# Kernel tuning notes

Hardware: AMD Instinct MI355X
Metric: run time of the kernel (lower is better)

The kernel has to match this reference:

```python
import jax, jax.numpy as jnp
import numpy as np

N_NODES = 50000
N_EDGES = 600000
N_GRAPHS = 1024
D = 128
NEG_SLOPE = 0.2


def _gat_conv(x, W, a_src, a_dst, b, src, dst, n):
    # PyG GATConv, heads=1, concat=True, add_self_loops=True (self loops
    # already appended to src/dst by the caller).
    h = x @ W                                  # [N, C]
    alpha_src = h @ a_src                      # [N]
    alpha_dst = h @ a_dst                      # [N]
    e = jax.nn.leaky_relu(alpha_src[src] + alpha_dst[dst], NEG_SLOPE)  # [E']
    # segment softmax over incoming edges of each destination node
    e_max = jax.ops.segment_max(e, dst, num_segments=n)
    ex = jnp.exp(e - e_max[dst])
    denom = jax.ops.segment_sum(ex, dst, num_segments=n)
    alpha = ex / denom[dst]
    out = jax.ops.segment_sum(h[src] * alpha[:, None], dst, num_segments=n)
    return out + b


def _global_mean_pool(x, batch, n_graphs):
    s = jax.ops.segment_sum(x, batch, num_segments=n_graphs)
    cnt = jax.ops.segment_sum(jnp.ones((x.shape[0],), x.dtype), batch,
                              num_segments=n_graphs)
    return s / jnp.maximum(cnt, 1.0)[:, None]


def setup_inputs() -> dict:
    key = jax.random.key(0)
    ks = jax.random.split(key, 12)
    x = jax.random.normal(ks[0], (N_NODES, D), dtype=jnp.float32)
    edge_index = jax.random.randint(ks[1], (2, N_EDGES), 0, N_NODES, dtype=jnp.int64)
    batch = jnp.sort(jax.random.randint(ks[2], (N_NODES,), 0, N_GRAPHS, dtype=jnp.int64))
    glorot = 1.0 / np.sqrt(D)
    return {
        "x": x,
        "edge_index": edge_index,
        "batch": batch,
        "W1": jax.random.normal(ks[3], (D, D), dtype=jnp.float32) * glorot,
        "att_src1": jax.random.normal(ks[4], (D,), dtype=jnp.float32) * glorot,
        "att_dst1": jax.random.normal(ks[5], (D,), dtype=jnp.float32) * glorot,
        "b1": jnp.zeros((D,), dtype=jnp.float32),
        "W2": jax.random.normal(ks[6], (D, D), dtype=jnp.float32) * glorot,
        "att_src2": jax.random.normal(ks[7], (D,), dtype=jnp.float32) * glorot,
        "att_dst2": jax.random.normal(ks[8], (D,), dtype=jnp.float32) * glorot,
        "b2": jnp.zeros((D,), dtype=jnp.float32),
    }


def reference(x, edge_index, batch, W1, att_src1, att_dst1, b1,
              W2, att_src2, att_dst2, b2):
    n = x.shape[0]
    loops = jnp.arange(n, dtype=edge_index.dtype)
    src = jnp.concatenate([edge_index[0], loops])
    dst = jnp.concatenate([edge_index[1], loops])

    h1 = jax.nn.relu(_gat_conv(x, W1, att_src1, att_dst1, b1, src, dst, n))
    emb1 = _global_mean_pool(h1, batch, N_GRAPHS)

    h2 = jax.nn.relu(_gat_conv(h1, W2, att_src2, att_dst2, b2, src, dst, n))
    emb2 = _global_mean_pool(h2, batch, N_GRAPHS)

    return (emb1, emb2)
```

## Files before the change

kernel.cpp:

```cpp
#include <hip/hip_runtime.h>
#include <hip/hip_fp16.h>
#include <cstdint>
#include <cstddef>

#define NN 50000
#define NE 600000
#define NT (NE + NN)
#define NG 1024
#define D 128
#define NEG_SLOPE 0.2f

typedef _Float16 half8 __attribute__((ext_vector_type(8)));
typedef float f32x4 __attribute__((ext_vector_type(4)));

__global__ void prep_misc(const float* __restrict__ W1, const float* __restrict__ W2,
                          _Float16* __restrict__ Wt1, _Float16* __restrict__ Wt2,
                          const int* __restrict__ batch, int* __restrict__ gptr,
                          unsigned* __restrict__ deg) {
    int i = blockIdx.x * 256 + threadIdx.x;
    if (i < NN) deg[i] = 0u;
    if (i < 2 * D * D) {
        const float* W  = (i < D * D) ? W1 : W2;
        _Float16*   Wt  = (i < D * D) ? Wt1 : Wt2;
        int j = i & (D * D - 1);
        int k = j >> 7, c = j & 127;
        Wt[c * D + k] = (_Float16)W[j];
    }
    if (i <= NG) {
        int lo = 0, hi = NN;
        while (lo < hi) { int mid = (lo + hi) >> 1; if (batch[mid] < i) lo = mid + 1; else hi = mid; }
        gptr[i] = lo;
    }
}

__global__ void hist_kernel(const int* __restrict__ ei1, unsigned* __restrict__ deg) {
    int e = blockIdx.x * blockDim.x + threadIdx.x;
    if (e >= NT) return;
    int d = (e < NE) ? ei1[e] : (e - NE);
    atomicAdd(deg + d, 1u);
}

__global__ void scan1(const unsigned* __restrict__ deg, unsigned* __restrict__ chunk,
                      unsigned* __restrict__ partials) {
    __shared__ unsigned sm[256];
    int i = blockIdx.x * 256 + threadIdx.x;
    unsigned v = (i < NN) ? deg[i] : 0u;
    sm[threadIdx.x] = v;
    __syncthreads();
    for (int off = 1; off < 256; off <<= 1) {
        unsigned t = (threadIdx.x >= off) ? sm[threadIdx.x - off] : 0u;
        __syncthreads();
        sm[threadIdx.x] += t;
        __syncthreads();
    }
    if (i < NN) chunk[i] = sm[threadIdx.x];
    if (threadIdx.x == 255) partials[blockIdx.x] = sm[255];
}

__global__ void scan2(unsigned* __restrict__ partials, int nb) {
    __shared__ unsigned sm[256];
    int i = threadIdx.x;
    sm[i] = (i < nb) ? partials[i] : 0u;
    __syncthreads();
    for (int off = 1; off < 256; off <<= 1) {
        unsigned t = (i >= off) ? sm[i - off] : 0u;
        __syncthreads();
        sm[i] += t;
        __syncthreads();
    }
    if (i < nb) partials[i] = sm[i];
}

__global__ void scan3(const unsigned* __restrict__ chunk, const unsigned* __restrict__ deg,
                      const unsigned* __restrict__ pscan, int* __restrict__ ptr,
                      int* __restrict__ fill) {
    int i = blockIdx.x * 256 + threadIdx.x;
    if (i < NN) {
        unsigned off = blockIdx.x ? pscan[blockIdx.x - 1] : 0u;
        int excl = (int)(chunk[i] - deg[i] + off);
        ptr[i] = excl;
        fill[i] = excl;
    }
    if (i == 0) ptr[NN] = NT;
}

__global__ void scatter_kernel(const int* __restrict__ ei0, const int* __restrict__ ei1,
                               int* __restrict__ fill, int* __restrict__ csr_src) {
    int e = blockIdx.x * blockDim.x + threadIdx.x;
    if (e >= NT) return;
    int s, d;
    if (e < NE) { s = ei0[e]; d = ei1[e]; } else { s = d = e - NE; }
    int pos = atomicAdd(fill + d, 1);
    csr_src[pos] = s;
}

template <bool FP16IN>
__global__ __launch_bounds__(256) void gemm_mfma(
    const void* __restrict__ Xv, const _Float16* __restrict__ Wt,
    const float* __restrict__ a_s, const float* __restrict__ a_d,
    __half2* __restrict__ Hh, float* __restrict__ AS, float* __restrict__ AD)
{
    __shared__ _Float16 Ht[64][132];
    int t = threadIdx.x;
    int w = t >> 6, lane = t & 63;
    int rowlane = lane & 15, kg = lane >> 4;
    int rb = (int)blockIdx.x * 64;
    int r0 = rb + w * 16;
    int r  = r0 + rowlane;
    int rc = r < NN ? r : NN - 1;

    half8 afr[4];
    if constexpr (FP16IN) {
        const _Float16* xr = (const _Float16*)Xv + (size_t)rc * D + kg * 8;
        #pragma unroll
        for (int kt = 0; kt < 4; ++kt)
            afr[kt] = *reinterpret_cast<const half8*>(xr + kt * 32);
    } else {
        const float* xr = (const float*)Xv + (size_t)rc * D + kg * 8;
        #pragma unroll
        for (int kt = 0; kt < 4; ++kt) {
            float4 u = *reinterpret_cast<const float4*>(xr + kt * 32);
            float4 v = *reinterpret_cast<const float4*>(xr + kt * 32 + 4);
            half8 a;
            a[0] = (_Float16)u.x; a[1] = (_Float16)u.y;
            a[2] = (_Float16)u.z; a[3] = (_Float16)u.w;
            a[4] = (_Float16)v.x; a[5] = (_Float16)v.y;
            a[6] = (_Float16)v.z; a[7] = (_Float16)v.w;
            afr[kt] = a;
        }
    }

    f32x4 acc[8];
    #pragma unroll
    for (int i = 0; i < 8; ++i) acc[i] = (f32x4){0.f, 0.f, 0.f, 0.f};

    const _Float16* wb = Wt + (size_t)rowlane * D + kg * 8;
    #pragma unroll
    for (int ct = 0; ct < 8; ++ct) {
        const _Float16* wc = wb + (size_t)ct * 16 * D;
        #pragma unroll
        for (int kt = 0; kt < 4; ++kt) {
            half8 b = *reinterpret_cast<const half8*>(wc + kt * 32);
            acc[ct] = __builtin_amdgcn_mfma_f32_16x16x32_f16(afr[kt], b, acc[ct], 0, 0, 0);
        }
    }

    float rs[4] = {0.f, 0.f, 0.f, 0.f}, rd[4] = {0.f, 0.f, 0.f, 0.f};
    #pragma unroll
    for (int ct = 0; ct < 8; ++ct) {
        float as_c = a_s[ct * 16 + rowlane];
        float ad_c = a_d[ct * 16 + rowlane];
        #pragma unroll
        for (int reg = 0; reg < 4; ++reg) {
            float v = acc[ct][reg];
            rs[reg] += v * as_c;
            rd[reg] += v * ad_c;
            Ht[w * 16 + kg * 4 + reg][ct * 16 + rowlane] = (_Float16)v;
        }
    }
    #pragma unroll
    for (int reg = 0; reg < 4; ++reg) {
        #pragma unroll
        for (int off = 1; off < 16; off <<= 1) {
            rs[reg] += __shfl_xor(rs[reg], off, 64);
            rd[reg] += __shfl_xor(rd[reg], off, 64);
        }
    }
    if (rowlane == 0) {
        #pragma unroll
        for (int reg = 0; reg < 4; ++reg) {
            int rr = r0 + kg * 4 + reg;
            if (rr < NN) { AS[rr] = rs[reg]; AD[rr] = rd[reg]; }
        }
    }
    __syncthreads();
    #pragma unroll
    for (int it = 0; it < 8; ++it) {
        int u = t + it * 256;
        int row = u >> 5, cu = u & 31;
        int g = rb + row;
        if (g < NN) {
            uint2 v = *reinterpret_cast<const uint2*>(&Ht[row][cu * 4]);
            *reinterpret_cast<uint2*>(Hh + (size_t)g * 64 + cu * 2) = v;
        }
    }
}

__device__ __forceinline__ void acc4(float w, uint2 v,
                                     float& a0, float& a1, float& a2, float& a3) {
    float2 lo = __half22float2(*reinterpret_cast<const __half2*>(&v.x));
    float2 hi = __half22float2(*reinterpret_cast<const __half2*>(&v.y));
    a0 += w * lo.x; a1 += w * lo.y; a2 += w * hi.x; a3 += w * hi.y;
}
__device__ __forceinline__ float shfl_f32(float v, int l) {
    return __shfl(v, l, 32);
}

__global__ __launch_bounds__(256) void gat_node(
    const int* __restrict__ ptr, const int* __restrict__ csr_src,
    const float* __restrict__ AS, const float* __restrict__ AD,
    const uint2* __restrict__ Hh, const float* __restrict__ B,
    uint2* __restrict__ HOUT)
{
    int wid  = (int)((blockIdx.x * blockDim.x + threadIdx.x) >> 6);
    int lane = threadIdx.x & 63;
    int l32  = lane & 31;
    int nid  = wid * 2 + (lane >> 5);
    if (nid >= NN) return;

    int beg = ptr[nid], end = ptr[nid + 1];
    int deg = end - beg;
    float ad_d = AD[nid];

    float m = -3.0e38f, den = 0.f;
    float a0 = 0.f, a1 = 0.f, a2 = 0.f, a3 = 0.f;
    const uint2* hb = Hh + l32;

    for (int c0 = 0; c0 < deg; c0 += 32) {
        int cnt = deg - c0; if (cnt > 32) cnt = 32;

        int   s_l = 0;
        float e_l = -3.0e38f;
        if (l32 < cnt) {
            s_l = csr_src[beg + c0 + l32];
            float e = AS[s_l] + ad_d;
            e_l = e > 0.f ? e : e * NEG_SLOPE;
        }
        float cm = e_l;
        #pragma unroll
        for (int off = 16; off; off >>= 1)
            cm = fmaxf(cm, __shfl_xor(cm, off, 32));
        float mn = fmaxf(m, cm);
        float w_l = (l32 < cnt) ? __expf(e_l - mn) : 0.f;
        float cs = w_l;
        #pragma unroll
        for (int off = 16; off; off >>= 1)
            cs += __shfl_xor(cs, off, 32);
        float f = __expf(m - mn);
        den = den * f + cs;
        a0 *= f; a1 *= f; a2 *= f; a3 *= f;
        m = mn;

        int j = 0;
        for (; j + 8 <= cnt; j += 8) {
            int   s0 = __shfl(s_l, j,     32);
            int   s1 = __shfl(s_l, j + 1, 32);
            int   s2 = __shfl(s_l, j + 2, 32);
            int   s3 = __shfl(s_l, j + 3, 32);
            int   s4 = __shfl(s_l, j + 4, 32);
            int   s5 = __shfl(s_l, j + 5, 32);
            int   s6 = __shfl(s_l, j + 6, 32);
            int   s7 = __shfl(s_l, j + 7, 32);
            float w0 = shfl_f32(w_l, j);
            float w1 = shfl_f32(w_l, j + 1);
            float w2 = shfl_f32(w_l, j + 2);
            float w3 = shfl_f32(w_l, j + 3);
            float w4 = shfl_f32(w_l, j + 4);
            float w5 = shfl_f32(w_l, j + 5);
            float w6 = shfl_f32(w_l, j + 6);
            float w7 = shfl_f32(w_l, j + 7);
            uint2 h0 = hb[(size_t)s0 * 32];
            uint2 h1 = hb[(size_t)s1 * 32];
            uint2 h2 = hb[(size_t)s2 * 32];
            uint2 h3 = hb[(size_t)s3 * 32];
            uint2 h4 = hb[(size_t)s4 * 32];
            uint2 h5 = hb[(size_t)s5 * 32];
            uint2 h6 = hb[(size_t)s6 * 32];
            uint2 h7 = hb[(size_t)s7 * 32];
            acc4(w0, h0, a0, a1, a2, a3);
            acc4(w1, h1, a0, a1, a2, a3);
            acc4(w2, h2, a0, a1, a2, a3);
            acc4(w3, h3, a0, a1, a2, a3);
            acc4(w4, h4, a0, a1, a2, a3);
            acc4(w5, h5, a0, a1, a2, a3);
            acc4(w6, h6, a0, a1, a2, a3);
            acc4(w7, h7, a0, a1, a2, a3);
        }
        for (; j + 4 <= cnt; j += 4) {
            int   s0 = __shfl(s_l, j,     32);
            int   s1 = __shfl(s_l, j + 1, 32);
            int   s2 = __shfl(s_l, j + 2, 32);
            int   s3 = __shfl(s_l, j + 3, 32);
            float w0 = shfl_f32(w_l, j);
            float w1 = shfl_f32(w_l, j + 1);
            float w2 = shfl_f32(w_l, j + 2);
            float w3 = shfl_f32(w_l, j + 3);
            uint2 h0 = hb[(size_t)s0 * 32];
            uint2 h1 = hb[(size_t)s1 * 32];
            uint2 h2 = hb[(size_t)s2 * 32];
            uint2 h3 = hb[(size_t)s3 * 32];
            acc4(w0, h0, a0, a1, a2, a3);
            acc4(w1, h1, a0, a1, a2, a3);
            acc4(w2, h2, a0, a1, a2, a3);
            acc4(w3, h3, a0, a1, a2, a3);
        }
        for (; j < cnt; ++j) {
            int   s0 = __shfl(s_l, j, 32);
            float w0 = shfl_f32(w_l, j);
            uint2 h0 = hb[(size_t)s0 * 32];
            acc4(w0, h0, a0, a1, a2, a3);
        }
    }

    float inv = 1.0f / den;
    float4 bv = *reinterpret_cast<const float4*>(B + l32 * 4);
    float o0 = fmaxf(a0 * inv + bv.x, 0.f);
    float o1 = fmaxf(a1 * inv + bv.y, 0.f);
    float o2 = fmaxf(a2 * inv + bv.z, 0.f);
    float o3 = fmaxf(a3 * inv + bv.w, 0.f);
    __half2 p0 = __floats2half2_rn(o0, o1);
    __half2 p1 = __floats2half2_rn(o2, o3);
    uint2 pv;
    pv.x = *reinterpret_cast<unsigned*>(&p0);
    pv.y = *reinterpret_cast<unsigned*>(&p1);
    HOUT[(size_t)nid * 32 + l32] = pv;
}

__global__ __launch_bounds__(128) void pool_kernel(
    const __half* __restrict__ houth, const int* __restrict__ gptr,
    float* __restrict__ OUT)
{
    int g = blockIdx.x, c = threadIdx.x;
    int lo = gptr[g], hi = gptr[g + 1];
    float s0 = 0.f, s1 = 0.f, s2 = 0.f, s3 = 0.f;
    int r = lo;
    for (; r + 4 <= hi; r += 4) {
        s0 += __half2float(houth[(size_t)(r + 0) * D + c]);
        s1 += __half2float(houth[(size_t)(r + 1) * D + c]);
        s2 += __half2float(houth[(size_t)(r + 2) * D + c]);
        s3 += __half2float(houth[(size_t)(r + 3) * D + c]);
    }
    for (; r < hi; ++r) s0 += __half2float(houth[(size_t)r * D + c]);
    float s = (s0 + s1) + (s2 + s3);
    float n = (float)(hi - lo);
    OUT[(size_t)g * D + c] = s / fmaxf(n, 1.f);
}

extern "C" void kernel_launch(void* const* d_in, const int* in_sizes, int n_in,
                              void* d_out, int out_size, void* d_ws, size_t ws_size,
                              hipStream_t stream)
{
    const float* x     = (const float*)d_in[0];
    const int*   ei    = (const int*)d_in[1];
    const int*   batch = (const int*)d_in[2];
    const float* W[2]    = { (const float*)d_in[3], (const float*)d_in[7] };
    const float* ASV[2]  = { (const float*)d_in[4], (const float*)d_in[8] };
    const float* ADV[2]  = { (const float*)d_in[5], (const float*)d_in[9] };
    const float* BV[2]   = { (const float*)d_in[6], (const float*)d_in[10] };
    float* out = (float*)d_out;
    float* ws  = (float*)d_ws;

    const int* ei0 = ei;
    const int* ei1 = ei + NE;

    const int NB = (NN + 255) / 256;

    size_t o = 0;
    unsigned* deg   = (unsigned*)(ws + o); o += NN;
    __half2*  Hh    = (__half2*)(ws + o);  o += (size_t)NN * 64;
    __half2*  houth = (__half2*)(ws + o);  o += (size_t)NN * 64;
    float*    asb   = ws + o;              o += NN;
    float*    adb   = ws + o;              o += NN;
    unsigned* chunk = (unsigned*)(ws + o); o += NN;
    int*      ptr   = (int*)(ws + o);      o += NN + 1;
    int*      fill  = (int*)(ws + o);      o += NN;
    int*      csr   = (int*)(ws + o);      o += NT;
    unsigned* parts = (unsigned*)(ws + o); o += 256;
    int*      gptr  = (int*)(ws + o);      o += NG + 1;
    _Float16* Wt1   = (_Float16*)(ws + o); o += (D * D) / 2;
    _Float16* Wt2   = (_Float16*)(ws + o); o += (D * D) / 2;

    const int edge_blocks = (NT + 255) / 256;
    const int gemm_blocks = (NN + 63) / 64;
    const int gat_blocks  = (NN / 2 + 3) / 4;

    prep_misc<<<NB, 256, 0, stream>>>(W[0], W[1], Wt1, Wt2, batch, gptr, deg);
    hist_kernel<<<edge_blocks, 256, 0, stream>>>(ei1, deg);
    scan1<<<NB, 256, 0, stream>>>(deg, chunk, parts);
    scan2<<<1, 256, 0, stream>>>(parts, NB);
    scan3<<<NB, 256, 0, stream>>>(chunk, deg, parts, ptr, fill);
    scatter_kernel<<<edge_blocks, 256, 0, stream>>>(ei0, ei1, fill, csr);

    gemm_mfma<false><<<gemm_blocks, 256, 0, stream>>>(x, Wt1, ASV[0], ADV[0],
                                                      Hh, asb, adb);
    gat_node<<<gat_blocks, 256, 0, stream>>>(ptr, csr, asb, adb, (const uint2*)Hh,
                                             BV[0], (uint2*)houth);
    pool_kernel<<<NG, 128, 0, stream>>>((const __half*)houth, gptr, out);

    gemm_mfma<true><<<gemm_blocks, 256, 0, stream>>>(houth, Wt2, ASV[1], ADV[1],
                                                     Hh, asb, adb);
    gat_node<<<gat_blocks, 256, 0, stream>>>(ptr, csr, asb, adb, (const uint2*)Hh,
                                             BV[1], (uint2*)houth);
    pool_kernel<<<NG, 128, 0, stream>>>((const __half*)houth, gptr, out + (size_t)NG * D);
}
```

Baseline: 204.3 us.

## Co-launch independent kernels and gather with 16 lanes per node

```diff
diff --git a/kernel.cpp b/kernel.cpp
--- a/kernel.cpp
+++ b/kernel.cpp
@@ -84,9 +84,11 @@
     if (i == 0) ptr[NN] = NT;
 }
 
-__global__ void scatter_kernel(const int* __restrict__ ei0, const int* __restrict__ ei1,
-                               int* __restrict__ fill, int* __restrict__ csr_src) {
-    int e = blockIdx.x * blockDim.x + threadIdx.x;
+__device__ __forceinline__ void scatter_body(int bid, const int* __restrict__ ei0,
+                                             const int* __restrict__ ei1,
+                                             int* __restrict__ fill,
+                                             int* __restrict__ csr_src) {
+    int e = bid * 256 + threadIdx.x;
     if (e >= NT) return;
     int s, d;
     if (e < NE) { s = ei0[e]; d = ei1[e]; } else { s = d = e - NE; }
@@ -95,8 +97,8 @@
 }
 
 template <bool FP16IN>
-__global__ __launch_bounds__(256) void gemm_mfma(
-    const void* __restrict__ Xv, const _Float16* __restrict__ Wt,
+__device__ __forceinline__ void gemm_body(
+    int bid, const void* __restrict__ Xv, const _Float16* __restrict__ Wt,
     const float* __restrict__ a_s, const float* __restrict__ a_d,
     __half2* __restrict__ Hh, float* __restrict__ AS, float* __restrict__ AD)
 {
@@ -104,7 +106,7 @@
     int t = threadIdx.x;
     int w = t >> 6, lane = t & 63;
     int rowlane = lane & 15, kg = lane >> 4;
-    int rb = (int)blockIdx.x * 64;
+    int rb = bid * 64;
     int r0 = rb + w * 16;
     int r  = r0 + rowlane;
     int rc = r < NN ? r : NN - 1;
@@ -186,141 +188,11 @@
     }
 }
 
-__device__ __forceinline__ void acc4(float w, uint2 v,
-                                     float& a0, float& a1, float& a2, float& a3) {
-    float2 lo = __half22float2(*reinterpret_cast<const __half2*>(&v.x));
-    float2 hi = __half22float2(*reinterpret_cast<const __half2*>(&v.y));
-    a0 += w * lo.x; a1 += w * lo.y; a2 += w * hi.x; a3 += w * hi.y;
-}
-__device__ __forceinline__ float shfl_f32(float v, int l) {
-    return __shfl(v, l, 32);
-}
-
-__global__ __launch_bounds__(256) void gat_node(
-    const int* __restrict__ ptr, const int* __restrict__ csr_src,
-    const float* __restrict__ AS, const float* __restrict__ AD,
-    const uint2* __restrict__ Hh, const float* __restrict__ B,
-    uint2* __restrict__ HOUT)
-{
-    int wid  = (int)((blockIdx.x * blockDim.x + threadIdx.x) >> 6);
-    int lane = threadIdx.x & 63;
-    int l32  = lane & 31;
-    int nid  = wid * 2 + (lane >> 5);
-    if (nid >= NN) return;
-
-    int beg = ptr[nid], end = ptr[nid + 1];
-    int deg = end - beg;
-    float ad_d = AD[nid];
-
-    float m = -3.0e38f, den = 0.f;
-    float a0 = 0.f, a1 = 0.f, a2 = 0.f, a3 = 0.f;
-    const uint2* hb = Hh + l32;
-
-    for (int c0 = 0; c0 < deg; c0 += 32) {
-        int cnt = deg - c0; if (cnt > 32) cnt = 32;
-
-        int   s_l = 0;
-        float e_l = -3.0e38f;
-        if (l32 < cnt) {
-            s_l = csr_src[beg + c0 + l32];
-            float e = AS[s_l] + ad_d;
-            e_l = e > 0.f ? e : e * NEG_SLOPE;
-        }
-        float cm = e_l;
-        #pragma unroll
-        for (int off = 16; off; off >>= 1)
-            cm = fmaxf(cm, __shfl_xor(cm, off, 32));
-        float mn = fmaxf(m, cm);
-        float w_l = (l32 < cnt) ? __expf(e_l - mn) : 0.f;
-        float cs = w_l;
-        #pragma unroll
-        for (int off = 16; off; off >>= 1)
-            cs += __shfl_xor(cs, off, 32);
-        float f = __expf(m - mn);
-        den = den * f + cs;
-        a0 *= f; a1 *= f; a2 *= f; a3 *= f;
-        m = mn;
-
-        int j = 0;
-        for (; j + 8 <= cnt; j += 8) {
-            int   s0 = __shfl(s_l, j,     32);
-            int   s1 = __shfl(s_l, j + 1, 32);
-            int   s2 = __shfl(s_l, j + 2, 32);
-            int   s3 = __shfl(s_l, j + 3, 32);
-            int   s4 = __shfl(s_l, j + 4, 32);
-            int   s5 = __shfl(s_l, j + 5, 32);
-            int   s6 = __shfl(s_l, j + 6, 32);
-            int   s7 = __shfl(s_l, j + 7, 32);
-            float w0 = shfl_f32(w_l, j);
-            float w1 = shfl_f32(w_l, j + 1);
-            float w2 = shfl_f32(w_l, j + 2);
-            float w3 = shfl_f32(w_l, j + 3);
-            float w4 = shfl_f32(w_l, j + 4);
-            float w5 = shfl_f32(w_l, j + 5);
-            float w6 = shfl_f32(w_l, j + 6);
-            float w7 = shfl_f32(w_l, j + 7);
-            uint2 h0 = hb[(size_t)s0 * 32];
-            uint2 h1 = hb[(size_t)s1 * 32];
-            uint2 h2 = hb[(size_t)s2 * 32];
-            uint2 h3 = hb[(size_t)s3 * 32];
-            uint2 h4 = hb[(size_t)s4 * 32];
-            uint2 h5 = hb[(size_t)s5 * 32];
-            uint2 h6 = hb[(size_t)s6 * 32];
-            uint2 h7 = hb[(size_t)s7 * 32];
-            acc4(w0, h0, a0, a1, a2, a3);
-            acc4(w1, h1, a0, a1, a2, a3);
-            acc4(w2, h2, a0, a1, a2, a3);
-            acc4(w3, h3, a0, a1, a2, a3);
-            acc4(w4, h4, a0, a1, a2, a3);
-            acc4(w5, h5, a0, a1, a2, a3);
-            acc4(w6, h6, a0, a1, a2, a3);
-            acc4(w7, h7, a0, a1, a2, a3);
-        }
-        for (; j + 4 <= cnt; j += 4) {
-            int   s0 = __shfl(s_l, j,     32);
-            int   s1 = __shfl(s_l, j + 1, 32);
-            int   s2 = __shfl(s_l, j + 2, 32);
-            int   s3 = __shfl(s_l, j + 3, 32);
-            float w0 = shfl_f32(w_l, j);
-            float w1 = shfl_f32(w_l, j + 1);
-            float w2 = shfl_f32(w_l, j + 2);
-            float w3 = shfl_f32(w_l, j + 3);
-            uint2 h0 = hb[(size_t)s0 * 32];
-            uint2 h1 = hb[(size_t)s1 * 32];
-            uint2 h2 = hb[(size_t)s2 * 32];
-            uint2 h3 = hb[(size_t)s3 * 32];
-            acc4(w0, h0, a0, a1, a2, a3);
-            acc4(w1, h1, a0, a1, a2, a3);
-            acc4(w2, h2, a0, a1, a2, a3);
-            acc4(w3, h3, a0, a1, a2, a3);
-        }
-        for (; j < cnt; ++j) {
-            int   s0 = __shfl(s_l, j, 32);
-            float w0 = shfl_f32(w_l, j);
-            uint2 h0 = hb[(size_t)s0 * 32];
-            acc4(w0, h0, a0, a1, a2, a3);
-        }
-    }
-
-    float inv = 1.0f / den;
-    float4 bv = *reinterpret_cast<const float4*>(B + l32 * 4);
-    float o0 = fmaxf(a0 * inv + bv.x, 0.f);
-    float o1 = fmaxf(a1 * inv + bv.y, 0.f);
-    float o2 = fmaxf(a2 * inv + bv.z, 0.f);
-    float o3 = fmaxf(a3 * inv + bv.w, 0.f);
-    __half2 p0 = __floats2half2_rn(o0, o1);
-    __half2 p1 = __floats2half2_rn(o2, o3);
-    uint2 pv;
-    pv.x = *reinterpret_cast<unsigned*>(&p0);
-    pv.y = *reinterpret_cast<unsigned*>(&p1);
-    HOUT[(size_t)nid * 32 + l32] = pv;
-}
-
-__global__ __launch_bounds__(128) void pool_kernel(
-    const __half* __restrict__ houth, const int* __restrict__ gptr,
-    float* __restrict__ OUT)
-{
-    int g = blockIdx.x, c = threadIdx.x;
+__device__ __forceinline__ void pool_body(int g, const __half* __restrict__ houth,
+                                          const int* __restrict__ gptr,
+                                          float* __restrict__ OUT) {
+    int c = threadIdx.x;
+    if (c >= 128) return;
     int lo = gptr[g], hi = gptr[g + 1];
     float s0 = 0.f, s1 = 0.f, s2 = 0.f, s3 = 0.f;
     int r = lo;
@@ -334,6 +206,168 @@
     float s = (s0 + s1) + (s2 + s3);
     float n = (float)(hi - lo);
     OUT[(size_t)g * D + c] = s / fmaxf(n, 1.f);
+}
+
+#define GEMM_BLOCKS 782
+#define EDGE_BLOCKS ((NT + 255) / 256)
+
+__global__ __launch_bounds__(256) void gemm1_scatter(
+    const float* __restrict__ x, const _Float16* __restrict__ Wt1,
+    const float* __restrict__ as1, const float* __restrict__ ad1,
+    __half2* __restrict__ Hh, float* __restrict__ AS, float* __restrict__ AD,
+    const int* __restrict__ ei0, const int* __restrict__ ei1,
+    int* __restrict__ fill, int* __restrict__ csr_src)
+{
+    int b = (int)blockIdx.x;
+    if (b < GEMM_BLOCKS) gemm_body<false>(b, x, Wt1, as1, ad1, Hh, AS, AD);
+    else                 scatter_body(b - GEMM_BLOCKS, ei0, ei1, fill, csr_src);
+}
+
+__global__ __launch_bounds__(256) void gemm2_pool1(
+    const void* __restrict__ houth, const _Float16* __restrict__ Wt2,
+    const float* __restrict__ as2, const float* __restrict__ ad2,
+    __half2* __restrict__ Hh, float* __restrict__ AS, float* __restrict__ AD,
+    const int* __restrict__ gptr, float* __restrict__ OUT)
+{
+    int b = (int)blockIdx.x;
+    if (b < GEMM_BLOCKS) gemm_body<true>(b, houth, Wt2, as2, ad2, Hh, AS, AD);
+    else                 pool_body(b - GEMM_BLOCKS, (const __half*)houth, gptr, OUT);
+}
+
+__global__ __launch_bounds__(256) void pool2_kernel(
+    const __half* __restrict__ houth, const int* __restrict__ gptr,
+    float* __restrict__ OUT)
+{
+    pool_body((int)blockIdx.x, houth, gptr, OUT);
+}
+
+__device__ __forceinline__ void acc8(float w, uint4 v, float* a) {
+    float2 p;
+    p = __half22float2(*reinterpret_cast<const __half2*>(&v.x)); a[0] += w * p.x; a[1] += w * p.y;
+    p = __half22float2(*reinterpret_cast<const __half2*>(&v.y)); a[2] += w * p.x; a[3] += w * p.y;
+    p = __half22float2(*reinterpret_cast<const __half2*>(&v.z)); a[4] += w * p.x; a[5] += w * p.y;
+    p = __half22float2(*reinterpret_cast<const __half2*>(&v.w)); a[6] += w * p.x; a[7] += w * p.y;
+}
+
+__global__ __launch_bounds__(256) void gat_node(
+    const int* __restrict__ ptr, const int* __restrict__ csr_src,
+    const float* __restrict__ AS, const float* __restrict__ AD,
+    const uint4* __restrict__ Hh, const float* __restrict__ B,
+    uint4* __restrict__ HOUT)
+{
+    int wid  = (int)((blockIdx.x * blockDim.x + threadIdx.x) >> 6);
+    int lane = threadIdx.x & 63;
+    int l16  = lane & 15;
+    int nid  = wid * 4 + (lane >> 4);
+    if (nid >= NN) return;
+
+    int beg = ptr[nid], end = ptr[nid + 1];
+    int deg = end - beg;
+    float ad_d = AD[nid];
+
+    float m = -3.0e38f, den = 0.f;
+    float a[8] = {0.f, 0.f, 0.f, 0.f, 0.f, 0.f, 0.f, 0.f};
+    const uint4* hb = Hh + l16;
+
+    for (int c0 = 0; c0 < deg; c0 += 16) {
+        int cnt = deg - c0; if (cnt > 16) cnt = 16;
+
+        int   s_l = 0;
+        float e_l = -3.0e38f;
+        if (l16 < cnt) {
+            s_l = csr_src[beg + c0 + l16];
+            float e = AS[s_l] + ad_d;
+            e_l = e > 0.f ? e : e * NEG_SLOPE;
+        }
+        float cm = e_l;
+        #pragma unroll
+        for (int off = 8; off; off >>= 1)
+            cm = fmaxf(cm, __shfl_xor(cm, off, 16));
+        float mn = fmaxf(m, cm);
+        float w_l = (l16 < cnt) ? __expf(e_l - mn) : 0.f;
+        float cs = w_l;
+        #pragma unroll
+        for (int off = 8; off; off >>= 1)
+            cs += __shfl_xor(cs, off, 16);
+        float f = __expf(m - mn);
+        den = den * f + cs;
+        #pragma unroll
+        for (int i = 0; i < 8; ++i) a[i] *= f;
+        m = mn;
+
+        int j = 0;
+        for (; j + 8 <= cnt; j += 8) {
+            int   s0 = __shfl(s_l, j,     16);
+            int   s1 = __shfl(s_l, j + 1, 16);
+            int   s2 = __shfl(s_l, j + 2, 16);
+            int   s3 = __shfl(s_l, j + 3, 16);
+            int   s4 = __shfl(s_l, j + 4, 16);
+            int   s5 = __shfl(s_l, j + 5, 16);
+            int   s6 = __shfl(s_l, j + 6, 16);
+            int   s7 = __shfl(s_l, j + 7, 16);
+            float w0 = __shfl(w_l, j,     16);
+            float w1 = __shfl(w_l, j + 1, 16);
+            float w2 = __shfl(w_l, j + 2, 16);
+            float w3 = __shfl(w_l, j + 3, 16);
+            float w4 = __shfl(w_l, j + 4, 16);
+            float w5 = __shfl(w_l, j + 5, 16);
+            float w6 = __shfl(w_l, j + 6, 16);
+            float w7 = __shfl(w_l, j + 7, 16);
+            uint4 h0 = hb[(size_t)s0 * 16];
+            uint4 h1 = hb[(size_t)s1 * 16];
+            uint4 h2 = hb[(size_t)s2 * 16];
+            uint4 h3 = hb[(size_t)s3 * 16];
+            uint4 h4 = hb[(size_t)s4 * 16];
+            uint4 h5 = hb[(size_t)s5 * 16];
+            uint4 h6 = hb[(size_t)s6 * 16];
+            uint4 h7 = hb[(size_t)s7 * 16];
+            acc8(w0, h0, a); acc8(w1, h1, a); acc8(w2, h2, a); acc8(w3, h3, a);
+            acc8(w4, h4, a); acc8(w5, h5, a); acc8(w6, h6, a); acc8(w7, h7, a);
+        }
+        for (; j + 4 <= cnt; j += 4) {
+            int   s0 = __shfl(s_l, j,     16);
+            int   s1 = __shfl(s_l, j + 1, 16);
+            int   s2 = __shfl(s_l, j + 2, 16);
+            int   s3 = __shfl(s_l, j + 3, 16);
+            float w0 = __shfl(w_l, j,     16);
+            float w1 = __shfl(w_l, j + 1, 16);
+            float w2 = __shfl(w_l, j + 2, 16);
+            float w3 = __shfl(w_l, j + 3, 16);
+            uint4 h0 = hb[(size_t)s0 * 16];
+            uint4 h1 = hb[(size_t)s1 * 16];
+            uint4 h2 = hb[(size_t)s2 * 16];
+            uint4 h3 = hb[(size_t)s3 * 16];
+            acc8(w0, h0, a); acc8(w1, h1, a); acc8(w2, h2, a); acc8(w3, h3, a);
+        }
+        for (; j < cnt; ++j) {
+            int   s0 = __shfl(s_l, j, 16);
+            float w0 = __shfl(w_l, j, 16);
+            uint4 h0 = hb[(size_t)s0 * 16];
+            acc8(w0, h0, a);
+        }
+    }
+
+    float inv = 1.0f / den;
+    float4 b0 = *reinterpret_cast<const float4*>(B + l16 * 8);
+    float4 b1 = *reinterpret_cast<const float4*>(B + l16 * 8 + 4);
+    float o0 = fmaxf(a[0] * inv + b0.x, 0.f);
+    float o1 = fmaxf(a[1] * inv + b0.y, 0.f);
+    float o2 = fmaxf(a[2] * inv + b0.z, 0.f);
+    float o3 = fmaxf(a[3] * inv + b0.w, 0.f);
+    float o4 = fmaxf(a[4] * inv + b1.x, 0.f);
+    float o5 = fmaxf(a[5] * inv + b1.y, 0.f);
+    float o6 = fmaxf(a[6] * inv + b1.z, 0.f);
+    float o7 = fmaxf(a[7] * inv + b1.w, 0.f);
+    __half2 p0 = __floats2half2_rn(o0, o1);
+    __half2 p1 = __floats2half2_rn(o2, o3);
+    __half2 p2 = __floats2half2_rn(o4, o5);
+    __half2 p3 = __floats2half2_rn(o6, o7);
+    uint4 pv;
+    pv.x = *reinterpret_cast<unsigned*>(&p0);
+    pv.y = *reinterpret_cast<unsigned*>(&p1);
+    pv.z = *reinterpret_cast<unsigned*>(&p2);
+    pv.w = *reinterpret_cast<unsigned*>(&p3);
+    HOUT[(size_t)nid * 16 + l16] = pv;
 }
 
 extern "C" void kernel_launch(void* const* d_in, const int* in_sizes, int n_in,
@@ -370,26 +404,24 @@
     _Float16* Wt1   = (_Float16*)(ws + o); o += (D * D) / 2;
     _Float16* Wt2   = (_Float16*)(ws + o); o += (D * D) / 2;
 
-    const int edge_blocks = (NT + 255) / 256;
-    const int gemm_blocks = (NN + 63) / 64;
-    const int gat_blocks  = (NN / 2 + 3) / 4;
+    const int gat_blocks = (NN / 4 + 3) / 4;
 
     prep_misc<<<NB, 256, 0, stream>>>(W[0], W[1], Wt1, Wt2, batch, gptr, deg);
-    hist_kernel<<<edge_blocks, 256, 0, stream>>>(ei1, deg);
+    hist_kernel<<<EDGE_BLOCKS, 256, 0, stream>>>(ei1, deg);
     scan1<<<NB, 256, 0, stream>>>(deg, chunk, parts);
     scan2<<<1, 256, 0, stream>>>(parts, NB);
     scan3<<<NB, 256, 0, stream>>>(chunk, deg, parts, ptr, fill);
-    scatter_kernel<<<edge_blocks, 256, 0, stream>>>(ei0, ei1, fill, csr);
-
-    gemm_mfma<false><<<gemm_blocks, 256, 0, stream>>>(x, Wt1, ASV[0], ADV[0],
-                                                      Hh, asb, adb);
-    gat_node<<<gat_blocks, 256, 0, stream>>>(ptr, csr, asb, adb, (const uint2*)Hh,
-                                             BV[0], (uint2*)houth);
-    pool_kernel<<<NG, 128, 0, stream>>>((const __half*)houth, gptr, out);
-
-    gemm_mfma<true><<<gemm_blocks, 256, 0, stream>>>(houth, Wt2, ASV[1], ADV[1],
-                                                     Hh, asb, adb);
-    gat_node<<<gat_blocks, 256, 0, stream>>>(ptr, csr, asb, adb, (const uint2*)Hh,
-                                             BV[1], (uint2*)houth);
-    pool_kernel<<<NG, 128, 0, stream>>>((const __half*)houth, gptr, out + (size_t)NG * D);
-}
+
+    gemm1_scatter<<<GEMM_BLOCKS + EDGE_BLOCKS, 256, 0, stream>>>(
+        x, Wt1, ASV[0], ADV[0], Hh, asb, adb, ei0, ei1, fill, csr);
+
+    gat_node<<<gat_blocks, 256, 0, stream>>>(ptr, csr, asb, adb, (const uint4*)Hh,
+                                             BV[0], (uint4*)houth);
+
+    gemm2_pool1<<<GEMM_BLOCKS + NG, 256, 0, stream>>>(
+        houth, Wt2, ASV[1], ADV[1], Hh, asb, adb, gptr, out);
+
+    gat_node<<<gat_blocks, 256, 0, stream>>>(ptr, csr, asb, adb, (const uint4*)Hh,
+                                             BV[1], (uint4*)houth);
+    pool2_kernel<<<NG, 256, 0, stream>>>((const __half*)houth, gptr, out + (size_t)NG * D);
+}
```

Result: slower. 210.1 us (+2.9%).
